# Optimization experiments

Hardware: AMD Instinct MI355X
Metric: run time of the kernel (lower is better)

Reference implementation:

```python
import jax, jax.numpy as jnp
import numpy as np

B, N, IN_DIM, DIM = 16, 512, 2048, 512
K, DEPTH, HEADS, DH, MLP, NC = 4, 2, 8, 64, 512, 10
INNER = HEADS * DH  # 512
TOPK = 2
TEMP = 1.0


def setup_inputs() -> dict:
    key = jax.random.key(0)
    ks = jax.random.split(key, 16)
    g = lambda i, shape, s=0.02: jax.random.normal(ks[i], shape, dtype=jnp.float32) * s
    z = lambda shape: jnp.zeros(shape, jnp.float32)
    o = lambda shape: jnp.ones(shape, jnp.float32)
    return {
        "x": jax.random.normal(ks[0], (B, N, IN_DIM), dtype=jnp.float32),
        "proj_w": g(1, (IN_DIM, DIM)),
        "proj_b": z((DIM,)),
        "qkv_w": g(2, (K, DEPTH, DIM, 3 * INNER)),
        "ao_w": g(3, (K, DEPTH, INNER, DIM)),
        "ao_b": z((K, DEPTH, DIM)),
        "ln1_g": o((K, DEPTH, DIM)),
        "ln1_b": z((K, DEPTH, DIM)),
        "ln2_g": o((K, DEPTH, DIM)),
        "ln2_b": z((K, DEPTH, DIM)),
        "mlp_w1": g(4, (K, DEPTH, DIM, MLP)),
        "mlp_b1": z((K, DEPTH, MLP)),
        "mlp_w2": g(5, (K, DEPTH, MLP, DIM)),
        "mlp_b2": z((K, DEPTH, DIM)),
        "lnf_g": o((K, DIM)),
        "lnf_b": z((K, DIM)),
        "router_w1": g(6, (DIM, 256)),
        "router_b1": z((256,)),
        "router_w2": g(7, (256, K)),
        "router_b2": z((K,)),
        "head_w1": g(8, (DIM, 128)),
        "head_b1": z((128,)),
        "head_w2": g(9, (128, NC)),
        "head_b2": z((NC,)),
    }


def _ln(x, g, b):
    m = x.mean(-1, keepdims=True)
    v = jnp.mean((x - m) ** 2, axis=-1, keepdims=True)
    return (x - m) * jax.lax.rsqrt(v + 1e-5) * g + b


def _expert(h, qkv_w, ao_w, ao_b, ln1g, ln1b, ln2g, ln2b, w1, b1, w2, b2, lnfg, lnfb):
    # h: [B, N, DIM]; pre-norm transformer, depth=DEPTH, then final LN + mean-pool.
    Bb, Nn, _ = h.shape
    scale = DH ** -0.5
    for l in range(DEPTH):
        y = _ln(h, ln1g[l], ln1b[l])
        q, k, v = jnp.split(y @ qkv_w[l], 3, axis=-1)
        q = q.reshape(Bb, Nn, HEADS, DH)
        k = k.reshape(Bb, Nn, HEADS, DH)
        v = v.reshape(Bb, Nn, HEADS, DH)
        att = jax.nn.softmax(jnp.einsum('bqhd,bkhd->bhqk', q, k) * scale, axis=-1)
        o = jnp.einsum('bhqk,bkhd->bqhd', att, v).reshape(Bb, Nn, INNER)
        h = h + o @ ao_w[l] + ao_b[l]
        y2 = _ln(h, ln2g[l], ln2b[l])
        h = h + jax.nn.gelu(y2 @ w1[l] + b1[l]) @ w2[l] + b2[l]
    return _ln(h, lnfg, lnfb).mean(1)  # [B, DIM]


def reference(x, proj_w, proj_b, qkv_w, ao_w, ao_b, ln1_g, ln1_b, ln2_g, ln2_b,
              mlp_w1, mlp_b1, mlp_w2, mlp_b2, lnf_g, lnf_b,
              router_w1, router_b1, router_w2, router_b2,
              head_w1, head_b1, head_w2, head_b2):
    # Shared projection (mode='shared')
    H = x @ proj_w + proj_b                       # [B, N, DIM]
    bag = H.mean(1)                               # [B, DIM]
    rl = jax.nn.relu(bag @ router_w1 + router_b1) @ router_w2 + router_b2
    g_soft = jax.nn.softmax(rl / TEMP, axis=-1)   # [B, K]
    vals, idx = jax.lax.top_k(g_soft, TOPK)
    w = vals / (vals.sum(-1, keepdims=True) + 1e-8)
    # Dense combine weights: [B, K], zero for non-selected experts.
    Wfull = (jax.nn.one_hot(idx, K, dtype=H.dtype) * w[..., None]).sum(1)
    latents = jnp.stack([
        _expert(H, qkv_w[e], ao_w[e], ao_b[e], ln1_g[e], ln1_b[e], ln2_g[e], ln2_b[e],
                mlp_w1[e], mlp_b1[e], mlp_w2[e], mlp_b2[e], lnf_g[e], lnf_b[e])
        for e in range(K)
    ])                                            # [K, B, DIM]
    z = jnp.einsum('kbd,bk->bd', latents, Wfull)  # weighted combine
    logits = jax.nn.relu(z @ head_w1 + head_b1) @ head_w2 + head_b2
    return (z, logits, g_soft)
```

## Files before the change

kernel.cpp:

```cpp
#include <hip/hip_runtime.h>
#include <math.h>

typedef unsigned short u16;
typedef unsigned int u32;
typedef float f32x4 __attribute__((ext_vector_type(4)));
typedef unsigned short u16x8 __attribute__((ext_vector_type(8)));
typedef unsigned short u16x4 __attribute__((ext_vector_type(4)));
typedef _Float16 f16x8 __attribute__((ext_vector_type(8)));

#define DEV static __device__ __forceinline__

constexpr int BB = 16, NN = 512, DIM = 512, DEP = 2;
constexpr long ROWS = (long)BB * NN;

DEV u16 f2h(float f){ _Float16 h = (_Float16)f; return __builtin_bit_cast(u16, h); }
DEV float h2f(u16 u){ return (float)__builtin_bit_cast(_Float16, u); }
DEV f32x4 mfma16h(u16x8 a, u16x8 b, f32x4 c){
  return __builtin_amdgcn_mfma_f32_16x16x32_f16(__builtin_bit_cast(f16x8, a), __builtin_bit_cast(f16x8, b), c, 0, 0, 0);
}
DEV u32 pkrtz(float a, float b){ auto r = __builtin_amdgcn_cvt_pkrtz(a, b); return __builtin_bit_cast(u32, r); }
DEV float gelu_f(float x){ return 0.5f * x * (1.f + tanhf(0.79788456080286536f * (x + 0.044715f * x * x * x))); }

DEV void gload16(const u16* g, u16* l){
  __builtin_amdgcn_global_load_lds((const __attribute__((address_space(1))) unsigned int*)(const void*)g,
                                   (__attribute__((address_space(3))) unsigned int*)(void*)l, 16, 0, 0);
}

DEV f32x4 vaddv(f32x4 a, f32x4 b){ f32x4 r; r[0]=a[0]+b[0]; r[1]=a[1]+b[1]; r[2]=a[2]+b[2]; r[3]=a[3]+b[3]; return r; }
DEV f32x4 shfl4(f32x4 v, int m){ f32x4 r; r[0]=__shfl_xor(v[0],m); r[1]=__shfl_xor(v[1],m); r[2]=__shfl_xor(v[2],m); r[3]=__shfl_xor(v[3],m); return r; }

__global__ __launch_bounds__(256) void castAll(const float* __restrict__ qkv_w, const float* __restrict__ ao_w,
                                               const float* __restrict__ mlp_w1, const float* __restrict__ mlp_w2,
                                               u16* __restrict__ WQ, u16* __restrict__ WAO,
                                               u16* __restrict__ W1t, u16* __restrict__ W2t)
{
  const int z = blockIdx.z;
  const float* src; u16* dst; int Nd;
  if (z < 8){ src = qkv_w + (long)z * 512 * 1536; dst = WQ + (long)z * 512 * 1536; Nd = 1536; }
  else {
    int m = (z - 8) >> 3, zz = (z - 8) & 7;
    src = (m == 0 ? ao_w : m == 1 ? mlp_w1 : mlp_w2) + (long)zz * 512 * 512;
    dst = (m == 0 ? WAO : m == 1 ? W1t : W2t) + (long)zz * 512 * 512;
    Nd = 512;
  }
  const int n0 = blockIdx.y * 32;
  if (n0 >= Nd) return;
  const int k0 = blockIdx.x * 32;
  __shared__ float t[32][33];
  const int r = threadIdx.x >> 5, cc = threadIdx.x & 31;
  #pragma unroll
  for (int i = 0; i < 4; i++) t[r + i * 8][cc] = src[(long)(k0 + r + i * 8) * Nd + n0 + cc];
  __syncthreads();
  #pragma unroll
  for (int i = 0; i < 4; i++) dst[(long)(n0 + r + i * 8) * 512 + k0 + cc] = f2h(t[cc][r + i * 8]);
}

__global__ __launch_bounds__(256) void castTp(const float* __restrict__ src, u16* __restrict__ dst)
{
  __shared__ float t[32][33];
  const int k0 = blockIdx.x * 32, n0 = blockIdx.y * 32;
  const int r = threadIdx.x >> 5, cc = threadIdx.x & 31;
  #pragma unroll
  for (int i = 0; i < 4; i++) t[r + i * 8][cc] = src[(long)(k0 + r + i * 8) * 512 + n0 + cc];
  __syncthreads();
  #pragma unroll
  for (int i = 0; i < 4; i++) dst[(long)(n0 + r + i * 8) * 2048 + k0 + cc] = f2h(t[cc][r + i * 8]);
}

__global__ __launch_bounds__(256) void xcast(const float* __restrict__ X, u16* __restrict__ Xf)
{
  long i0 = ((long)blockIdx.x * 256 + threadIdx.x) * 8;
  f32x4 v0 = *(const f32x4*)(X + i0), v1 = *(const f32x4*)(X + i0 + 4);
  u16x8 hh;
  hh[0] = f2h(v0[0]); hh[1] = f2h(v0[1]); hh[2] = f2h(v0[2]); hh[3] = f2h(v0[3]);
  hh[4] = f2h(v1[0]); hh[5] = f2h(v1[1]); hh[6] = f2h(v1[2]); hh[7] = f2h(v1[3]);
  *(u16x8*)(Xf + i0) = hh;
}

__global__ __launch_bounds__(256) void gemm_proj(const u16* __restrict__ Xf, const u16* __restrict__ WP,
                                                 const float* __restrict__ bias, u16* __restrict__ Hout)
{
  const int mt = blockIdx.x, nt = blockIdx.y;
  __shared__ __align__(16) u16 As[64 * 64], Bs[128 * 64];
  const int tid = threadIdx.x, lane = tid & 63, wv = tid >> 6;
  const int wm = wv >> 1, wn = wv & 1, l4 = lane >> 4, l15 = lane & 15;
  const long a0 = (long)(mt * 64) * 2048, b0 = (long)(nt * 128) * 2048;
  const int srow = tid >> 3, sslot = tid & 7;
  f32x4 zero = {0.f, 0.f, 0.f, 0.f};
  f32x4 acc[2][4];
  #pragma unroll
  for (int mi = 0; mi < 2; mi++)
    #pragma unroll
    for (int ni = 0; ni < 4; ni++) acc[mi][ni] = zero;

  for (int kt = 0; kt < 2048; kt += 64){
    #pragma unroll
    for (int p = 0; p < 2; p++){
      int r = p * 32 + srow;
      int sg = sslot ^ (r & 7);
      gload16(Xf + a0 + (long)r * 2048 + kt + sg * 8, As + p * 2048 + wv * 512);
    }
    #pragma unroll
    for (int p = 0; p < 4; p++){
      int r = p * 32 + srow;
      int sg = sslot ^ (r & 7);
      gload16(WP + b0 + (long)r * 2048 + kt + sg * 8, Bs + p * 2048 + wv * 512);
    }
    __syncthreads();
    #pragma unroll
    for (int ks = 0; ks < 2; ks++){
      u16x8 af[2], bfr[4];
      #pragma unroll
      for (int mi = 0; mi < 2; mi++){
        int ra = wm * 32 + mi * 16 + l15;
        af[mi] = *(const u16x8*)(As + ra * 64 + ((((ks << 2) | l4)) ^ (ra & 7)) * 8);
      }
      #pragma unroll
      for (int ni = 0; ni < 4; ni++){
        int rb = wn * 64 + ni * 16 + l15;
        bfr[ni] = *(const u16x8*)(Bs + rb * 64 + ((((ks << 2) | l4)) ^ (rb & 7)) * 8);
      }
      #pragma unroll
      for (int mi = 0; mi < 2; mi++)
        #pragma unroll
        for (int ni = 0; ni < 4; ni++)
          acc[mi][ni] = mfma16h(af[mi], bfr[ni], acc[mi][ni]);
    }
    __syncthreads();
  }
  #pragma unroll
  for (int mi = 0; mi < 2; mi++)
    #pragma unroll
    for (int ni = 0; ni < 4; ni++){
      const int gr0 = mt * 64 + wm * 32 + mi * 16 + l4 * 4;
      const int gc = nt * 128 + wn * 64 + ni * 16 + l15;
      float bb = bias[gc];
      #pragma unroll
      for (int i = 0; i < 4; i++) Hout[(long)(gr0 + i) * 512 + gc] = f2h(acc[mi][ni][i] + bb);
    }
}

template<int EPI>
__global__ __launch_bounds__(256) void gemm_bt(const u16* __restrict__ A, int K, long sAe,
                                               const u16* __restrict__ Bt, long sBe,
                                               const float* __restrict__ bias, int sBiasE,
                                               u16* __restrict__ Cout, long sCe, int N,
                                               const int* __restrict__ pairs,
                                               const u16* __restrict__ resin)
{
  const int pe = pairs[blockIdx.x >> 2];
  const int e = pe >> 4, bb = pe & 15;
  const int row0 = bb * 512 + (blockIdx.x & 3) * 128;
  const int nt = blockIdx.y;
  A += (long)e * sAe + (long)row0 * K;
  Bt += (long)e * sBe + (long)(nt * 128) * K;
  const float* bias_e = bias ? bias + (long)e * sBiasE : nullptr;

  __shared__ __align__(16) u16 As[128 * 64];
  __shared__ __align__(16) u16 Bs[128 * 64];
  const int tid = threadIdx.x, lane = tid & 63, wv = tid >> 6;
  const int wm = wv >> 1, wn = wv & 1, l4 = lane >> 4, l15 = lane & 15;
  const int srow = tid >> 3, sslot = tid & 7;
  f32x4 zero = {0.f, 0.f, 0.f, 0.f};
  f32x4 acc[4][4];
  #pragma unroll
  for (int mi = 0; mi < 4; mi++)
    #pragma unroll
    for (int ni = 0; ni < 4; ni++) acc[mi][ni] = zero;

  for (int kt = 0; kt < K; kt += 64){
    #pragma unroll
    for (int p = 0; p < 4; p++){
      int r = p * 32 + srow;
      int sg = sslot ^ (r & 7);
      long go = (long)r * K + kt + sg * 8;
      int lo = p * 2048 + wv * 512;
      gload16(A + go, As + lo);
      gload16(Bt + go, Bs + lo);
    }
    __syncthreads();
    #pragma unroll
    for (int ks = 0; ks < 2; ks++){
      u16x8 af[4], bfr[4];
      #pragma unroll
      for (int mi = 0; mi < 4; mi++){
        int ra = wm * 64 + mi * 16 + l15;
        af[mi] = *(const u16x8*)(As + ra * 64 + ((((ks << 2) | l4)) ^ (ra & 7)) * 8);
      }
      #pragma unroll
      for (int ni = 0; ni < 4; ni++){
        int rb = wn * 64 + ni * 16 + l15;
        bfr[ni] = *(const u16x8*)(Bs + rb * 64 + ((((ks << 2) | l4)) ^ (rb & 7)) * 8);
      }
      #pragma unroll
      for (int mi = 0; mi < 4; mi++)
        #pragma unroll
        for (int ni = 0; ni < 4; ni++)
          acc[mi][ni] = mfma16h(af[mi], bfr[ni], acc[mi][ni]);
    }
    __syncthreads();
  }

  #pragma unroll
  for (int mi = 0; mi < 4; mi++)
    #pragma unroll
    for (int ni = 0; ni < 4; ni++){
      const int gr0 = row0 + wm * 64 + mi * 16 + l4 * 4;
      const int gc = nt * 128 + wn * 64 + ni * 16 + l15;
      float bb2 = bias_e ? bias_e[gc] : 0.f;
      #pragma unroll
      for (int i = 0; i < 4; i++){
        float val = acc[mi][ni][i] + bb2;
        long idx = (long)e * sCe + (long)(gr0 + i) * N + gc;
        if (EPI == 0){
          Cout[idx] = f2h(val);
        } else if (EPI == 1){
          Cout[idx] = f2h(gelu_f(val));
        } else if (EPI == 2){
          Cout[idx] = f2h(h2f(Cout[idx]) + val);
        } else {
          Cout[idx] = f2h(h2f(resin[(long)(gr0 + i) * N + gc]) + val);
        }
      }
    }
}

__global__ __launch_bounds__(256) void attn(const u16* __restrict__ qkv, u16* __restrict__ obf, const int* __restrict__ pairs)
{
  const int pe = pairs[blockIdx.x & 31];
  const int e = pe >> 4, b = pe & 15;
  const int hh = (blockIdx.x >> 5) & 7;
  const int qt = blockIdx.x >> 8;
  const u16* base = qkv + ((long)e * ROWS + (long)b * NN) * 1536;

  __shared__ u16 Ks[64 * 72];
  __shared__ u16 Vts[64 * 72];
  __shared__ u16 Ps[4][32 * 72];
  __shared__ float Lq[4][32];
  const int tid = threadIdx.x, lane = tid & 63, wv = tid >> 6;
  const int l4 = lane >> 4, l15 = lane & 15;
  const int qr0 = qt * 128 + wv * 32;
  constexpr float CSC = 0.125f * 1.44269504088896340736f;

  u16x8 qf[2][2];
  #pragma unroll
  for (int mi = 0; mi < 2; mi++)
    #pragma unroll
    for (int ks = 0; ks < 2; ks++){
      u16x8 raw = *(const u16x8*)(base + (long)(qr0 + mi * 16 + l15) * 1536 + hh * 64 + ks * 32 + l4 * 8);
      #pragma unroll
      for (int j = 0; j < 8; j++) qf[mi][ks][j] = f2h(h2f(raw[j]) * CSC);
    }

  f32x4 zero = {0.f, 0.f, 0.f, 0.f};
  f32x4 o[2][4]; float lrun[2] = {0.f, 0.f};
  #pragma unroll
  for (int mi = 0; mi < 2; mi++)
    #pragma unroll
    for (int df = 0; df < 4; df++) o[mi][df] = zero;
  const int sr = tid >> 3, ss = tid & 7;

  for (int c = 0; c < 8; c++){
    const int kk0 = c * 64;
    u16x8 kv0 = *(const u16x8*)(base + (long)(kk0 + sr) * 1536 + 512 + hh * 64 + ss * 8);
    u16x8 kv1 = *(const u16x8*)(base + (long)(kk0 + sr + 32) * 1536 + 512 + hh * 64 + ss * 8);
    u16x8 vv0 = *(const u16x8*)(base + (long)(kk0 + sr) * 1536 + 1024 + hh * 64 + ss * 8);
    u16x8 vv1 = *(const u16x8*)(base + (long)(kk0 + sr + 32) * 1536 + 1024 + hh * 64 + ss * 8);
    __syncthreads();
    *(u16x8*)(Ks + sr * 72 + ss * 8) = kv0;
    *(u16x8*)(Ks + (sr + 32) * 72 + ss * 8) = kv1;
    #pragma unroll
    for (int j = 0; j < 8; j++){
      int d = ss * 8 + j;
      Vts[d * 72 + (sr ^ (ss * 8))] = vv0[j];
      Vts[d * 72 + ((sr + 32) ^ (ss * 8))] = vv1[j];
    }
    __syncthreads();

    u16x8 kf[4][2];
    #pragma unroll
    for (int n = 0; n < 4; n++)
      #pragma unroll
      for (int ks = 0; ks < 2; ks++)
        kf[n][ks] = *(const u16x8*)(Ks + (n * 16 + l15) * 72 + ks * 32 + l4 * 8);

    f32x4 sv[2][4];
    __builtin_amdgcn_s_setprio(1);
    #pragma unroll
    for (int mi = 0; mi < 2; mi++)
      #pragma unroll
      for (int n = 0; n < 4; n++){
        sv[mi][n] = zero;
        sv[mi][n] = mfma16h(kf[n][0], qf[mi][0], sv[mi][n]);
        sv[mi][n] = mfma16h(kf[n][1], qf[mi][1], sv[mi][n]);
      }
    __builtin_amdgcn_s_setprio(0);

    #pragma unroll
    for (int mi = 0; mi < 2; mi++){
      float lp = 0.f;
      #pragma unroll
      for (int n = 0; n < 4; n++){
        float p0 = __builtin_amdgcn_exp2f(sv[mi][n][0]);
        float p1 = __builtin_amdgcn_exp2f(sv[mi][n][1]);
        float p2 = __builtin_amdgcn_exp2f(sv[mi][n][2]);
        float p3 = __builtin_amdgcn_exp2f(sv[mi][n][3]);
        lp += (p0 + p1) + (p2 + p3);
        union { u32 w[2]; u16x4 h; } pk;
        pk.w[0] = pkrtz(p0, p1);
        pk.w[1] = pkrtz(p2, p3);
        *(u16x4*)(&Ps[wv][(mi * 16 + l15) * 72 + n * 16 + l4 * 4]) = pk.h;
      }
      lp += __shfl_xor(lp, 16);
      lp += __shfl_xor(lp, 32);
      lrun[mi] += lp;
    }

    u16x8 pf[2][2], vf[4][2];
    #pragma unroll
    for (int mi = 0; mi < 2; mi++)
      #pragma unroll
      for (int k2 = 0; k2 < 2; k2++)
        pf[mi][k2] = *(const u16x8*)(&Ps[wv][(mi * 16 + l15) * 72 + k2 * 32 + l4 * 8]);
    #pragma unroll
    for (int df = 0; df < 4; df++)
      #pragma unroll
      for (int k2 = 0; k2 < 2; k2++){
        int d = df * 16 + l15;
        int swz = ((d >> 3) & 7) * 8;
        vf[df][k2] = *(const u16x8*)(Vts + d * 72 + ((k2 * 32 + l4 * 8) ^ swz));
      }
    __builtin_amdgcn_s_setprio(1);
    #pragma unroll
    for (int mi = 0; mi < 2; mi++)
      #pragma unroll
      for (int df = 0; df < 4; df++){
        o[mi][df] = mfma16h(pf[mi][0], vf[df][0], o[mi][df]);
        o[mi][df] = mfma16h(pf[mi][1], vf[df][1], o[mi][df]);
      }
    __builtin_amdgcn_s_setprio(0);
  }

  if (l4 == 0){
    Lq[wv][l15] = lrun[0];
    Lq[wv][16 + l15] = lrun[1];
  }
  __syncthreads();
  #pragma unroll
  for (int mi = 0; mi < 2; mi++){
    f32x4 inv;
    #pragma unroll
    for (int i = 0; i < 4; i++) inv[i] = 1.f / Lq[wv][mi * 16 + l4 * 4 + i];
    #pragma unroll
    for (int df = 0; df < 4; df++)
      #pragma unroll
      for (int i = 0; i < 4; i++)
        obf[(long)e * ROWS * DIM + (long)(b * NN + qr0 + mi * 16 + l4 * 4 + i) * DIM + hh * 64 + df * 16 + l15]
          = f2h(o[mi][df][i] * inv[i]);
  }
}

__global__ __launch_bounds__(256) void ln_rows(const u16* __restrict__ hin, long sHe,
                                               const float* __restrict__ g, const float* __restrict__ bta,
                                               int sGE, u16* __restrict__ outb, const int* __restrict__ pairs)
{
  const int pe = pairs[blockIdx.x >> 7];
  const int e = pe >> 4;
  const int tid = threadIdx.x, lane = tid & 63, wv = tid >> 6;
  const int row = (pe & 15) * 512 + ((blockIdx.x & 127) << 2) + wv;
  const u16* x = hin + (long)e * sHe + (long)row * DIM + lane * 8;
  u16x8 vh = *(const u16x8*)x;
  float v[8];
  #pragma unroll
  for (int j = 0; j < 8; j++) v[j] = h2f(vh[j]);
  float s = 0.f, sq = 0.f;
  #pragma unroll
  for (int j = 0; j < 8; j++){ s += v[j]; sq += v[j] * v[j]; }
  #pragma unroll
  for (int m = 32; m >= 1; m >>= 1){ s += __shfl_xor(s, m); sq += __shfl_xor(sq, m); }
  float mean = s * (1.f / DIM); float var = sq * (1.f / DIM) - mean * mean;
  float inv = rsqrtf(var + 1e-5f);
  const float* ge = g + (long)e * sGE + lane * 8;
  const float* be = bta + (long)e * sGE + lane * 8;
  f32x4 g0 = *(const f32x4*)ge, g1 = *(const f32x4*)(ge + 4);
  f32x4 b0 = *(const f32x4*)be, b1 = *(const f32x4*)(be + 4);
  u16x8 yo;
  #pragma unroll
  for (int j = 0; j < 4; j++) yo[j] = f2h((v[j] - mean) * inv * g0[j] + b0[j]);
  #pragma unroll
  for (int j = 0; j < 4; j++) yo[4 + j] = f2h((v[4 + j] - mean) * inv * g1[j] + b1[j]);
  *(u16x8*)(outb + ((long)e * ROWS + row) * DIM + lane * 8) = yo;
}

__global__ __launch_bounds__(512) void bag_partial(const u16* __restrict__ H, float* __restrict__ bagp)
{
  const int b = blockIdx.x, c = blockIdx.y;
  const int tid = threadIdx.x;
  const u16* r = H + ((long)b * 512 + c * 64) * DIM + tid;
  float s = 0.f;
  #pragma unroll 8
  for (int n = 0; n < 64; n++) s += h2f(r[n * DIM]);
  bagp[((long)c * BB + b) * DIM + tid] = s;
}

__global__ __launch_bounds__(256) void router_mm(const float* __restrict__ bagp, const float* __restrict__ rw1,
                                                 float* __restrict__ hidp)
{
  const int kc = blockIdx.x, b = blockIdx.y;
  const int tid = threadIdx.x;
  __shared__ float bs[64];
  if (tid < 64){
    int k = kc * 64 + tid;
    float s = 0.f;
    #pragma unroll
    for (int c = 0; c < 8; c++) s += bagp[((long)c * BB + b) * DIM + k];
    bs[tid] = s * (1.f / NN);
  }
  __syncthreads();
  float a = 0.f;
  #pragma unroll 8
  for (int k = 0; k < 64; k++) a += bs[k] * rw1[(long)(kc * 64 + k) * 256 + tid];
  hidp[((long)b * 8 + kc) * 256 + tid] = a;
}

__global__ __launch_bounds__(256) void router_fin(const float* __restrict__ hidp,
                                                  const float* __restrict__ rb1,
                                                  const float* __restrict__ rw2, const float* __restrict__ rb2,
                                                  float* __restrict__ gout, float* __restrict__ wexp, int* __restrict__ pairs)
{
  const int b = blockIdx.x;
  const int tid = threadIdx.x, lane = tid & 63, wv = tid >> 6;
  __shared__ f32x4 red2[4];
  float a = rb1[tid];
  #pragma unroll
  for (int kc = 0; kc < 8; kc++) a += hidp[((long)b * 8 + kc) * 256 + tid];
  float h = fmaxf(a, 0.f);
  f32x4 w4 = *(const f32x4*)(rw2 + tid * 4);
  f32x4 s = {h * w4[0], h * w4[1], h * w4[2], h * w4[3]};
  s = vaddv(s, shfl4(s, 1)); s = vaddv(s, shfl4(s, 2)); s = vaddv(s, shfl4(s, 4));
  s = vaddv(s, shfl4(s, 8)); s = vaddv(s, shfl4(s, 16)); s = vaddv(s, shfl4(s, 32));
  if (lane == 0) red2[wv] = s;
  __syncthreads();
  if (tid == 0){
    f32x4 lg = vaddv(vaddv(red2[0], red2[1]), vaddv(red2[2], red2[3]));
    float l4a[4]; float m = -3e38f;
    #pragma unroll
    for (int k = 0; k < 4; k++){ l4a[k] = lg[k] + rb2[k]; m = fmaxf(m, l4a[k]); }
    float ex[4]; float ssum2 = 0;
    #pragma unroll
    for (int k = 0; k < 4; k++){ ex[k] = expf(l4a[k] - m); ssum2 += ex[k]; }
    float gv[4];
    #pragma unroll
    for (int k = 0; k < 4; k++){ gv[k] = ex[k] / ssum2; gout[b * 4 + k] = gv[k]; }
    int i0 = 0; float v0 = gv[0];
    #pragma unroll
    for (int k = 1; k < 4; k++) if (gv[k] > v0){ v0 = gv[k]; i0 = k; }
    int i1 = -1; float v1 = -1.f;
    #pragma unroll
    for (int k = 0; k < 4; k++) if (k != i0 && gv[k] > v1){ v1 = gv[k]; i1 = k; }
    float den = v0 + v1 + 1e-8f;
    #pragma unroll
    for (int k = 0; k < 4; k++) wexp[k * BB + b] = (k == i0) ? (v0 / den) : ((k == i1) ? (v1 / den) : 0.f);
    pairs[2 * b]     = (i0 << 4) | b;
    pairs[2 * b + 1] = (i1 << 4) | b;
  }
}

__global__ __launch_bounds__(512) void lnf_partial(const u16* __restrict__ hin, const float* __restrict__ g,
                                                   const float* __restrict__ bta, float* __restrict__ part,
                                                   const int* __restrict__ pairs)
{
  const int p = blockIdx.x, chunk = blockIdx.y;
  const int pe = pairs[p];
  const int e = pe >> 4, b = pe & 15;
  const int tid = threadIdx.x, lane = tid & 63, wv = tid >> 6;
  __shared__ float gs[512], bsh[512];
  gs[tid] = g[e * DIM + tid]; bsh[tid] = bta[e * DIM + tid];
  __syncthreads();
  float acc[8] = {0, 0, 0, 0, 0, 0, 0, 0};
  #pragma unroll
  for (int i = 0; i < 8; i++){
    int n = chunk * 64 + i * 8 + wv;
    const u16* r = hin + ((long)e * ROWS + (long)b * NN + n) * DIM + lane * 8;
    u16x8 vh = *(const u16x8*)r;
    float v[8];
    #pragma unroll
    for (int j = 0; j < 8; j++) v[j] = h2f(vh[j]);
    float s = 0, sq = 0;
    #pragma unroll
    for (int j = 0; j < 8; j++){ s += v[j]; sq += v[j] * v[j]; }
    #pragma unroll
    for (int m = 32; m >= 1; m >>= 1){ s += __shfl_xor(s, m); sq += __shfl_xor(sq, m); }
    float mean = s * (1.f / DIM), var = sq * (1.f / DIM) - mean * mean, inv = rsqrtf(var + 1e-5f);
    #pragma unroll
    for (int j = 0; j < 8; j++) acc[j] += (v[j] - mean) * inv * gs[lane * 8 + j] + bsh[lane * 8 + j];
  }
  __shared__ float red[8][512];
  #pragma unroll
  for (int j = 0; j < 8; j++) red[wv][lane * 8 + j] = acc[j];
  __syncthreads();
  float ssum = 0;
  #pragma unroll
  for (int w = 0; w < 8; w++) ssum += red[w][tid];
  part[((long)p * 8 + chunk) * 512 + tid] = ssum;
}

__global__ __launch_bounds__(512) void lnf_fin(const float* __restrict__ part, float* __restrict__ latents,
                                               const int* __restrict__ pairs)
{
  const int p = blockIdx.x;
  const int pe = pairs[p];
  const int e = pe >> 4, b = pe & 15;
  const int tid = threadIdx.x;
  float s = 0.f;
  #pragma unroll
  for (int c = 0; c < 8; c++) s += part[((long)p * 8 + c) * 512 + tid];
  latents[((long)e * BB + b) * DIM + tid] = s * (1.f / NN);
}

__global__ __launch_bounds__(128) void head_l1(const float* __restrict__ latents, const float* __restrict__ wexp,
                                               const float* __restrict__ hw1, float* __restrict__ out,
                                               float* __restrict__ hidp2)
{
  const int b = blockIdx.x, kc = blockIdx.y;
  const int tid = threadIdx.x;
  __shared__ float zs[128];
  float wk[4];
  #pragma unroll
  for (int k = 0; k < 4; k++) wk[k] = wexp[k * BB + b];
  int c = kc * 128 + tid;
  float z = 0.f;
  #pragma unroll
  for (int k = 0; k < 4; k++) if (wk[k] != 0.f) z += wk[k] * latents[((long)k * BB + b) * DIM + c];
  zs[tid] = z;
  out[b * 512 + c] = z;
  __syncthreads();
  float a = 0.f;
  #pragma unroll 8
  for (int cc = 0; cc < 128; cc++) a += zs[cc] * hw1[(long)(kc * 128 + cc) * 128 + tid];
  hidp2[((long)b * 4 + kc) * 128 + tid] = a;
}

__global__ __launch_bounds__(128) void head_fin(const float* __restrict__ hidp2, const float* __restrict__ hb1,
                                                const float* __restrict__ hw2, const float* __restrict__ hb2,
                                                float* __restrict__ out)
{
  const int b = blockIdx.x;
  const int tid = threadIdx.x;
  __shared__ float hid[128];
  float h = hb1[tid];
  #pragma unroll
  for (int kc = 0; kc < 4; kc++) h += hidp2[((long)b * 4 + kc) * 128 + tid];
  hid[tid] = fmaxf(h, 0.f);
  __syncthreads();
  if (tid < 10){
    float s = hb2[tid];
    #pragma unroll 16
    for (int j = 0; j < 128; j++) s += hid[j] * hw2[j * 10 + tid];
    out[8192 + b * 10 + tid] = s;
  }
}

extern "C" void kernel_launch(void* const* d_in, const int* in_sizes, int n_in,
                              void* d_out, int out_size, void* d_ws, size_t ws_size,
                              hipStream_t stream)
{
  const float* x      = (const float*)d_in[0];
  const float* proj_w = (const float*)d_in[1];
  const float* proj_b = (const float*)d_in[2];
  const float* qkv_w  = (const float*)d_in[3];
  const float* ao_w   = (const float*)d_in[4];
  const float* ao_b   = (const float*)d_in[5];
  const float* ln1_g  = (const float*)d_in[6];
  const float* ln1_b  = (const float*)d_in[7];
  const float* ln2_g  = (const float*)d_in[8];
  const float* ln2_b  = (const float*)d_in[9];
  const float* mlp_w1 = (const float*)d_in[10];
  const float* mlp_b1 = (const float*)d_in[11];
  const float* mlp_w2 = (const float*)d_in[12];
  const float* mlp_b2 = (const float*)d_in[13];
  const float* lnf_g  = (const float*)d_in[14];
  const float* lnf_b  = (const float*)d_in[15];
  const float* rw1    = (const float*)d_in[16];
  const float* rb1    = (const float*)d_in[17];
  const float* rw2    = (const float*)d_in[18];
  const float* rb2    = (const float*)d_in[19];
  const float* hw1    = (const float*)d_in[20];
  const float* hb1    = (const float*)d_in[21];
  const float* hw2    = (const float*)d_in[22];
  const float* hb2    = (const float*)d_in[23];
  float* out = (float*)d_out;

  char* base = (char*)d_ws; size_t off = 0;
  auto alloc = [&](size_t bytes) -> void* { void* p = base + off; off = (off + bytes + 255) & ~(size_t)255; return p; };

  u16* WQ   = (u16*)alloc((size_t)8 * 1536 * 512 * 2);
  u16* WAO  = (u16*)alloc((size_t)8 * 512 * 512 * 2);
  u16* W1t  = (u16*)alloc((size_t)8 * 512 * 512 * 2);
  u16* W2t  = (u16*)alloc((size_t)8 * 512 * 512 * 2);
  u16* WP   = (u16*)alloc((size_t)512 * 2048 * 2);
  u16* HF   = (u16*)alloc((size_t)ROWS * 512 * 2);
  u16* HH   = (u16*)alloc((size_t)4 * ROWS * 512 * 2);
  u16* YB   = (u16*)alloc((size_t)4 * ROWS * 512 * 2);
  u16* QKVb = (u16*)alloc((size_t)4 * ROWS * 1536 * 2);
  float* WEXP = (float*)alloc(64 * 4);
  int* PAIRS  = (int*)alloc(32 * 4);
  float* LAT  = (float*)alloc(4 * 16 * 512 * 4);
  float* BAGP = (float*)alloc((size_t)8 * 16 * 512 * 4);
  float* HIDP = (float*)alloc((size_t)16 * 8 * 256 * 4);
  float* PART = (float*)alloc((size_t)32 * 8 * 512 * 4);
  float* HIDP2 = (float*)alloc((size_t)16 * 4 * 128 * 4);
  u16* Y2B = QKVb;
  u16* TB  = QKVb + (size_t)4 * ROWS * 512;
  u16* OB  = YB;
  u16* Xf  = QKVb;

  castAll<<<dim3(16, 48, 32), 256, 0, stream>>>(qkv_w, ao_w, mlp_w1, mlp_w2, WQ, WAO, W1t, W2t);
  castTp<<<dim3(64, 16), 256, 0, stream>>>(proj_w, WP);
  xcast<<<8192, 256, 0, stream>>>(x, Xf);

  gemm_proj<<<dim3(128, 4), 256, 0, stream>>>(Xf, WP, proj_b, HF);
  bag_partial<<<dim3(16, 8), 512, 0, stream>>>(HF, BAGP);
  router_mm<<<dim3(8, 16), 256, 0, stream>>>(BAGP, rw1, HIDP);
  router_fin<<<16, 256, 0, stream>>>(HIDP, rb1, rw2, rb2, out + 8192 + 160, WEXP, PAIRS);

  for (int l = 0; l < 2; l++){
    if (l == 0)
      ln_rows<<<4096, 256, 0, stream>>>(HF, 0L, ln1_g, ln1_b, DEP * 512, YB, PAIRS);
    else
      ln_rows<<<4096, 256, 0, stream>>>(HH, ROWS * 512, ln1_g + 512, ln1_b + 512, DEP * 512, YB, PAIRS);
    gemm_bt<0><<<dim3(128, 12), 256, 0, stream>>>(YB, 512, ROWS * 512, WQ + (long)l * 1536 * 512, (long)DEP * 1536 * 512,
                                                  nullptr, 0, QKVb, ROWS * 1536, 1536, PAIRS, nullptr);
    attn<<<1024, 256, 0, stream>>>(QKVb, OB, PAIRS);
    if (l == 0)
      gemm_bt<3><<<dim3(128, 4), 256, 0, stream>>>(OB, 512, ROWS * 512, WAO, (long)DEP * 512 * 512,
                                                   ao_b, DEP * 512, HH, ROWS * 512, 512, PAIRS, HF);
    else
      gemm_bt<2><<<dim3(128, 4), 256, 0, stream>>>(OB, 512, ROWS * 512, WAO + (long)512 * 512, (long)DEP * 512 * 512,
                                                   ao_b + 512, DEP * 512, HH, ROWS * 512, 512, PAIRS, nullptr);
    ln_rows<<<4096, 256, 0, stream>>>(HH, ROWS * 512, ln2_g + l * 512, ln2_b + l * 512, DEP * 512, Y2B, PAIRS);
    gemm_bt<1><<<dim3(128, 4), 256, 0, stream>>>(Y2B, 512, ROWS * 512, W1t + (long)l * 512 * 512, (long)DEP * 512 * 512,
                                                 mlp_b1 + l * 512, DEP * 512, TB, ROWS * 512, 512, PAIRS, nullptr);
    gemm_bt<2><<<dim3(128, 4), 256, 0, stream>>>(TB, 512, ROWS * 512, W2t + (long)l * 512 * 512, (long)DEP * 512 * 512,
                                                 mlp_b2 + l * 512, DEP * 512, HH, ROWS * 512, 512, PAIRS, nullptr);
  }

  lnf_partial<<<dim3(32, 8), 512, 0, stream>>>(HH, lnf_g, lnf_b, PART, PAIRS);
  lnf_fin<<<32, 512, 0, stream>>>(PART, LAT, PAIRS);
  head_l1<<<dim3(16, 4), 128, 0, stream>>>(LAT, WEXP, hw1, out, HIDP2);
  head_fin<<<16, 128, 0, stream>>>(HIDP2, hb1, hw2, hb2, out);
}
```

Before: 430.2 us.

## Swap MFMA operands for vectorized epilogue stores and use 64-row tiles for N=512 GEMMs

```diff
diff --git a/kernel.cpp b/kernel.cpp
--- a/kernel.cpp
+++ b/kernel.cpp
@@ -7,6 +7,7 @@
 typedef unsigned short u16x8 __attribute__((ext_vector_type(8)));
 typedef unsigned short u16x4 __attribute__((ext_vector_type(4)));
 typedef _Float16 f16x8 __attribute__((ext_vector_type(8)));
+typedef _Float16 f16x4 __attribute__((ext_vector_type(4)));
 
 #define DEV static __device__ __forceinline__
 
@@ -19,6 +20,7 @@
   return __builtin_amdgcn_mfma_f32_16x16x32_f16(__builtin_bit_cast(f16x8, a), __builtin_bit_cast(f16x8, b), c, 0, 0, 0);
 }
 DEV u32 pkrtz(float a, float b){ auto r = __builtin_amdgcn_cvt_pkrtz(a, b); return __builtin_bit_cast(u32, r); }
+DEV u16x4 cvt4(f32x4 a){ f16x4 h = {(_Float16)a[0], (_Float16)a[1], (_Float16)a[2], (_Float16)a[3]}; return __builtin_bit_cast(u16x4, h); }
 DEV float gelu_f(float x){ return 0.5f * x * (1.f + tanhf(0.79788456080286536f * (x + 0.044715f * x * x * x))); }
 
 DEV void gload16(const u16* g, u16* l){
@@ -124,7 +126,7 @@
       for (int mi = 0; mi < 2; mi++)
         #pragma unroll
         for (int ni = 0; ni < 4; ni++)
-          acc[mi][ni] = mfma16h(af[mi], bfr[ni], acc[mi][ni]);
+          acc[mi][ni] = mfma16h(bfr[ni], af[mi], acc[mi][ni]);
     }
     __syncthreads();
   }
@@ -132,15 +134,15 @@
   for (int mi = 0; mi < 2; mi++)
     #pragma unroll
     for (int ni = 0; ni < 4; ni++){
-      const int gr0 = mt * 64 + wm * 32 + mi * 16 + l4 * 4;
-      const int gc = nt * 128 + wn * 64 + ni * 16 + l15;
-      float bb = bias[gc];
-      #pragma unroll
-      for (int i = 0; i < 4; i++) Hout[(long)(gr0 + i) * 512 + gc] = f2h(acc[mi][ni][i] + bb);
-    }
-}
-
-template<int EPI>
+      const int grow = mt * 64 + wm * 32 + mi * 16 + l15;
+      const int gc0 = nt * 128 + wn * 64 + ni * 16 + l4 * 4;
+      f32x4 bb = *(const f32x4*)(bias + gc0);
+      f32x4 a = vaddv(acc[mi][ni], bb);
+      *(u16x4*)(Hout + (long)grow * 512 + gc0) = cvt4(a);
+    }
+}
+
+template<int EPI, int MT>
 __global__ __launch_bounds__(256) void gemm_bt(const u16* __restrict__ A, int K, long sAe,
                                                const u16* __restrict__ Bt, long sBe,
                                                const float* __restrict__ bias, int sBiasE,
@@ -148,43 +150,48 @@
                                                const int* __restrict__ pairs,
                                                const u16* __restrict__ resin)
 {
-  const int pe = pairs[blockIdx.x >> 2];
+  constexpr int MI = MT / 32;
+  constexpr int PSH = (MT == 128) ? 2 : 3;
+  const int pe = pairs[blockIdx.x >> PSH];
   const int e = pe >> 4, bb = pe & 15;
-  const int row0 = bb * 512 + (blockIdx.x & 3) * 128;
+  const int row0 = bb * 512 + (blockIdx.x & ((1 << PSH) - 1)) * MT;
   const int nt = blockIdx.y;
   A += (long)e * sAe + (long)row0 * K;
   Bt += (long)e * sBe + (long)(nt * 128) * K;
   const float* bias_e = bias ? bias + (long)e * sBiasE : nullptr;
 
-  __shared__ __align__(16) u16 As[128 * 64];
+  __shared__ __align__(16) u16 As[MT * 64];
   __shared__ __align__(16) u16 Bs[128 * 64];
   const int tid = threadIdx.x, lane = tid & 63, wv = tid >> 6;
   const int wm = wv >> 1, wn = wv & 1, l4 = lane >> 4, l15 = lane & 15;
   const int srow = tid >> 3, sslot = tid & 7;
   f32x4 zero = {0.f, 0.f, 0.f, 0.f};
-  f32x4 acc[4][4];
-  #pragma unroll
-  for (int mi = 0; mi < 4; mi++)
+  f32x4 acc[MI][4];
+  #pragma unroll
+  for (int mi = 0; mi < MI; mi++)
     #pragma unroll
     for (int ni = 0; ni < 4; ni++) acc[mi][ni] = zero;
 
   for (int kt = 0; kt < K; kt += 64){
+    #pragma unroll
+    for (int p = 0; p < MI; p++){
+      int r = p * 32 + srow;
+      int sg = sslot ^ (r & 7);
+      gload16(A + (long)r * K + kt + sg * 8, As + p * 2048 + wv * 512);
+    }
     #pragma unroll
     for (int p = 0; p < 4; p++){
       int r = p * 32 + srow;
       int sg = sslot ^ (r & 7);
-      long go = (long)r * K + kt + sg * 8;
-      int lo = p * 2048 + wv * 512;
-      gload16(A + go, As + lo);
-      gload16(Bt + go, Bs + lo);
+      gload16(Bt + (long)r * K + kt + sg * 8, Bs + p * 2048 + wv * 512);
     }
     __syncthreads();
     #pragma unroll
     for (int ks = 0; ks < 2; ks++){
-      u16x8 af[4], bfr[4];
-      #pragma unroll
-      for (int mi = 0; mi < 4; mi++){
-        int ra = wm * 64 + mi * 16 + l15;
+      u16x8 af[MI], bfr[4];
+      #pragma unroll
+      for (int mi = 0; mi < MI; mi++){
+        int ra = wm * (MT / 2) + mi * 16 + l15;
         af[mi] = *(const u16x8*)(As + ra * 64 + ((((ks << 2) | l4)) ^ (ra & 7)) * 8);
       }
       #pragma unroll
@@ -193,34 +200,45 @@
         bfr[ni] = *(const u16x8*)(Bs + rb * 64 + ((((ks << 2) | l4)) ^ (rb & 7)) * 8);
       }
       #pragma unroll
-      for (int mi = 0; mi < 4; mi++)
+      for (int mi = 0; mi < MI; mi++)
         #pragma unroll
         for (int ni = 0; ni < 4; ni++)
-          acc[mi][ni] = mfma16h(af[mi], bfr[ni], acc[mi][ni]);
+          acc[mi][ni] = mfma16h(bfr[ni], af[mi], acc[mi][ni]);
     }
     __syncthreads();
   }
 
   #pragma unroll
-  for (int mi = 0; mi < 4; mi++)
+  for (int mi = 0; mi < MI; mi++)
     #pragma unroll
     for (int ni = 0; ni < 4; ni++){
-      const int gr0 = row0 + wm * 64 + mi * 16 + l4 * 4;
-      const int gc = nt * 128 + wn * 64 + ni * 16 + l15;
-      float bb2 = bias_e ? bias_e[gc] : 0.f;
-      #pragma unroll
-      for (int i = 0; i < 4; i++){
-        float val = acc[mi][ni][i] + bb2;
-        long idx = (long)e * sCe + (long)(gr0 + i) * N + gc;
-        if (EPI == 0){
-          Cout[idx] = f2h(val);
-        } else if (EPI == 1){
-          Cout[idx] = f2h(gelu_f(val));
-        } else if (EPI == 2){
-          Cout[idx] = f2h(h2f(Cout[idx]) + val);
-        } else {
-          Cout[idx] = f2h(h2f(resin[(long)(gr0 + i) * N + gc]) + val);
-        }
+      const int grow = row0 + wm * (MT / 2) + mi * 16 + l15;
+      const int gc0 = nt * 128 + wn * 64 + ni * 16 + l4 * 4;
+      f32x4 a = acc[mi][ni];
+      if (bias_e){
+        f32x4 bb2 = *(const f32x4*)(bias_e + gc0);
+        a = vaddv(a, bb2);
+      }
+      long idx = (long)e * sCe + (long)grow * N + gc0;
+      if (EPI == 0){
+        *(u16x4*)(Cout + idx) = cvt4(a);
+      } else if (EPI == 1){
+        f32x4 gg;
+        #pragma unroll
+        for (int i = 0; i < 4; i++) gg[i] = gelu_f(a[i]);
+        *(u16x4*)(Cout + idx) = cvt4(gg);
+      } else if (EPI == 2){
+        u16x4 old = *(const u16x4*)(Cout + idx);
+        f32x4 r;
+        #pragma unroll
+        for (int i = 0; i < 4; i++) r[i] = h2f(old[i]) + a[i];
+        *(u16x4*)(Cout + idx) = cvt4(r);
+      } else {
+        u16x4 old = *(const u16x4*)(resin + (long)grow * N + gc0);
+        f32x4 r;
+        #pragma unroll
+        for (int i = 0; i < 4; i++) r[i] = h2f(old[i]) + a[i];
+        *(u16x4*)(Cout + idx) = cvt4(r);
       }
     }
 }
@@ -236,7 +254,6 @@
   __shared__ u16 Ks[64 * 72];
   __shared__ u16 Vts[64 * 72];
   __shared__ u16 Ps[4][32 * 72];
-  __shared__ float Lq[4][32];
   const int tid = threadIdx.x, lane = tid & 63, wv = tid >> 6;
   const int l4 = lane >> 4, l15 = lane & 15;
   const int qr0 = qt * 128 + wv * 32;
@@ -335,28 +352,23 @@
     for (int mi = 0; mi < 2; mi++)
       #pragma unroll
       for (int df = 0; df < 4; df++){
-        o[mi][df] = mfma16h(pf[mi][0], vf[df][0], o[mi][df]);
-        o[mi][df] = mfma16h(pf[mi][1], vf[df][1], o[mi][df]);
+        o[mi][df] = mfma16h(vf[df][0], pf[mi][0], o[mi][df]);
+        o[mi][df] = mfma16h(vf[df][1], pf[mi][1], o[mi][df]);
       }
     __builtin_amdgcn_s_setprio(0);
   }
 
-  if (l4 == 0){
-    Lq[wv][l15] = lrun[0];
-    Lq[wv][16 + l15] = lrun[1];
-  }
-  __syncthreads();
   #pragma unroll
   for (int mi = 0; mi < 2; mi++){
-    f32x4 inv;
-    #pragma unroll
-    for (int i = 0; i < 4; i++) inv[i] = 1.f / Lq[wv][mi * 16 + l4 * 4 + i];
-    #pragma unroll
-    for (int df = 0; df < 4; df++)
-      #pragma unroll
-      for (int i = 0; i < 4; i++)
-        obf[(long)e * ROWS * DIM + (long)(b * NN + qr0 + mi * 16 + l4 * 4 + i) * DIM + hh * 64 + df * 16 + l15]
-          = f2h(o[mi][df][i] * inv[i]);
+    float inv = 1.f / lrun[mi];
+    long rb = (long)e * ROWS * DIM + (long)(b * NN + qr0 + mi * 16 + l15) * DIM + hh * 64;
+    #pragma unroll
+    for (int df = 0; df < 4; df++){
+      f32x4 a;
+      #pragma unroll
+      for (int i = 0; i < 4; i++) a[i] = o[mi][df][i] * inv;
+      *(u16x4*)(obf + rb + df * 16 + l4 * 4) = cvt4(a);
+    }
   }
 }
 
@@ -629,20 +641,20 @@
       ln_rows<<<4096, 256, 0, stream>>>(HF, 0L, ln1_g, ln1_b, DEP * 512, YB, PAIRS);
     else
       ln_rows<<<4096, 256, 0, stream>>>(HH, ROWS * 512, ln1_g + 512, ln1_b + 512, DEP * 512, YB, PAIRS);
-    gemm_bt<0><<<dim3(128, 12), 256, 0, stream>>>(YB, 512, ROWS * 512, WQ + (long)l * 1536 * 512, (long)DEP * 1536 * 512,
-                                                  nullptr, 0, QKVb, ROWS * 1536, 1536, PAIRS, nullptr);
+    gemm_bt<0, 128><<<dim3(128, 12), 256, 0, stream>>>(YB, 512, ROWS * 512, WQ + (long)l * 1536 * 512, (long)DEP * 1536 * 512,
+                                                       nullptr, 0, QKVb, ROWS * 1536, 1536, PAIRS, nullptr);
     attn<<<1024, 256, 0, stream>>>(QKVb, OB, PAIRS);
     if (l == 0)
-      gemm_bt<3><<<dim3(128, 4), 256, 0, stream>>>(OB, 512, ROWS * 512, WAO, (long)DEP * 512 * 512,
-                                                   ao_b, DEP * 512, HH, ROWS * 512, 512, PAIRS, HF);
+      gemm_bt<3, 64><<<dim3(256, 4), 256, 0, stream>>>(OB, 512, ROWS * 512, WAO, (long)DEP * 512 * 512,
+                                                       ao_b, DEP * 512, HH, ROWS * 512, 512, PAIRS, HF);
     else
-      gemm_bt<2><<<dim3(128, 4), 256, 0, stream>>>(OB, 512, ROWS * 512, WAO + (long)512 * 512, (long)DEP * 512 * 512,
-                                                   ao_b + 512, DEP * 512, HH, ROWS * 512, 512, PAIRS, nullptr);
+      gemm_bt<2, 64><<<dim3(256, 4), 256, 0, stream>>>(OB, 512, ROWS * 512, WAO + (long)512 * 512, (long)DEP * 512 * 512,
+                                                       ao_b + 512, DEP * 512, HH, ROWS * 512, 512, PAIRS, nullptr);
     ln_rows<<<4096, 256, 0, stream>>>(HH, ROWS * 512, ln2_g + l * 512, ln2_b + l * 512, DEP * 512, Y2B, PAIRS);
-    gemm_bt<1><<<dim3(128, 4), 256, 0, stream>>>(Y2B, 512, ROWS * 512, W1t + (long)l * 512 * 512, (long)DEP * 512 * 512,
-                                                 mlp_b1 + l * 512, DEP * 512, TB, ROWS * 512, 512, PAIRS, nullptr);
-    gemm_bt<2><<<dim3(128, 4), 256, 0, stream>>>(TB, 512, ROWS * 512, W2t + (long)l * 512 * 512, (long)DEP * 512 * 512,
-                                                 mlp_b2 + l * 512, DEP * 512, HH, ROWS * 512, 512, PAIRS, nullptr);
+    gemm_bt<1, 64><<<dim3(256, 4), 256, 0, stream>>>(Y2B, 512, ROWS * 512, W1t + (long)l * 512 * 512, (long)DEP * 512 * 512,
+                                                     mlp_b1 + l * 512, DEP * 512, TB, ROWS * 512, 512, PAIRS, nullptr);
+    gemm_bt<2, 64><<<dim3(256, 4), 256, 0, stream>>>(TB, 512, ROWS * 512, W2t + (long)l * 512 * 512, (long)DEP * 512 * 512,
+                                                     mlp_b2 + l * 512, DEP * 512, HH, ROWS * 512, 512, PAIRS, nullptr);
   }
 
   lnf_partial<<<dim3(32, 8), 512, 0, stream>>>(HH, lnf_g, lnf_b, PART, PAIRS);
```

Result: no change. 435.1 us (+1.1%).
